# Kernel tuning notes

Hardware: AMD Instinct MI355X
Metric: run time of the kernel (lower is better)

Reference implementation:

```python
import jax, jax.numpy as jnp
from jax import lax
import numpy as np

B = 128          # batch (matches module BATCH_SIZE)
H = W = 64       # image size
E = 8            # num_experts
K = 2            # top_k
C = 1000         # num_classes (expert hidden_size)
D = 14 * 14 * 64 # flattened conv features: 64->62->31->29->14


def setup_inputs() -> dict:
    key = jax.random.key(0)
    ks = jax.random.split(key, 10)
    return {
        "x": jax.random.normal(ks[0], (B, H, W, 1), dtype=jnp.float32),
        "conv1_w": jax.random.normal(ks[1], (3, 3, 1, 32), dtype=jnp.float32) * 0.05,
        "conv1_b": jnp.zeros((32,), dtype=jnp.float32),
        "conv2_w": jax.random.normal(ks[2], (3, 3, 32, 64), dtype=jnp.float32) * 0.05,
        "conv2_b": jnp.zeros((64,), dtype=jnp.float32),
        "gate_w": jax.random.normal(ks[3], (D, E), dtype=jnp.float32) * 0.001,
        "gate_b": jnp.zeros((E,), dtype=jnp.float32),
        "expert_w": jax.random.normal(ks[4], (E, D, C), dtype=jnp.float32) * 0.001,
        "expert_b": jnp.zeros((E, C), dtype=jnp.float32),
    }


def _conv_relu(x, w, b):
    y = lax.conv_general_dilated(x, w, window_strides=(1, 1), padding="VALID",
                                 dimension_numbers=("NHWC", "HWIO", "NHWC"))
    return jax.nn.relu(y + b)


def _maxpool2(x):
    return lax.reduce_window(x, -jnp.inf, lax.max,
                             (1, 2, 2, 1), (1, 2, 2, 1), "VALID")


def reference(x, conv1_w, conv1_b, conv2_w, conv2_b, gate_w, gate_b, expert_w, expert_b):
    # conv block (dropout is identity at inference)
    h = _maxpool2(_conv_relu(x, conv1_w, conv1_b))
    h = _maxpool2(_conv_relu(h, conv2_w, conv2_b))
    h = h.reshape(h.shape[0], -1)                       # [B, D]

    # gating: softmax + top-k
    gates = jax.nn.softmax(h @ gate_w + gate_b)         # [B, E]
    topk_w, topk_i = lax.top_k(gates, K)                # [B, K]

    # all experts (tiny dense layers stacked), then gather top-k and combine
    expert_out = jnp.einsum("bd,edc->bec", h, expert_w) + expert_b  # [B, E, C]
    sel = jnp.take_along_axis(expert_out, topk_i[:, :, None], axis=1)  # [B, K, C]
    combined = jnp.sum(sel * topk_w[:, :, None], axis=1)              # [B, C]

    return jax.nn.softmax(combined)
```

## Files before the change

### kernel.cpp

```cpp
#include <hip/hip_runtime.h>
#include <math.h>

#define D_FEAT 12544
#define NC 1000
#define RB 16
#define S4 32
#define DSLICE 392
#define NIT (DSLICE/4)
#define CT2 500

__global__ __launch_bounds__(256) void k1_conv1(
    const float* __restrict__ x, const float* __restrict__ w,
    const float* __restrict__ bias, float* __restrict__ h1,
    int* __restrict__ cnt)
{
    if (blockIdx.x == 0 && threadIdx.x < 8) cnt[threadIdx.x] = 0;

    int co  = threadIdx.x & 31;
    int pxi = threadIdx.x >> 5;
    int blk = blockIdx.x;
    int pxg = blk & 3;
    int py  = (blk >> 2) % 31;
    int b   = blk / (31 * 4);
    int px  = pxg * 8 + pxi;
    if (px >= 31) return;

    float wr[9];
#pragma unroll
    for (int t = 0; t < 9; ++t) wr[t] = w[t * 32 + co];
    float bb = bias[co];

    float in[4][4];
    const float* xb = x + ((size_t)(b * 64 + 2 * py) * 64 + 2 * px);
#pragma unroll
    for (int r = 0; r < 4; ++r)
#pragma unroll
        for (int c = 0; c < 4; ++c)
            in[r][c] = xb[r * 64 + c];

    float a00 = 0.f, a01 = 0.f, a10 = 0.f, a11 = 0.f;
#pragma unroll
    for (int ky = 0; ky < 3; ++ky)
#pragma unroll
        for (int kx = 0; kx < 3; ++kx) {
            float wv = wr[ky * 3 + kx];
            a00 = fmaf(in[ky][kx],     wv, a00);
            a01 = fmaf(in[ky][kx + 1], wv, a01);
            a10 = fmaf(in[ky + 1][kx], wv, a10);
            a11 = fmaf(in[ky + 1][kx + 1], wv, a11);
        }
    a00 = fmaxf(a00 + bb, 0.f);
    a01 = fmaxf(a01 + bb, 0.f);
    a10 = fmaxf(a10 + bb, 0.f);
    a11 = fmaxf(a11 + bb, 0.f);
    float v = fmaxf(fmaxf(a00, a01), fmaxf(a10, a11));
    h1[((size_t)(b * 31 + py) * 31 + px) * 32 + co] = v;
}

__global__ __launch_bounds__(448) void k2_conv2(
    const float* __restrict__ h1, const float* __restrict__ w2,
    const float* __restrict__ b2, float* __restrict__ h)
{
    __shared__ float wl[9 * 32 * 32];

    int co  = threadIdx.x & 31;
    int px  = threadIdx.x >> 5;
    int blk = blockIdx.x;
    int cob = blk & 1;
    int py  = (blk >> 1) % 14;
    int b   = blk / 28;

    for (int i = threadIdx.x; i < 9 * 32 * 32; i += 448) {
        int tapci = i >> 5;
        int col   = i & 31;
        wl[i] = w2[tapci * 64 + cob * 32 + col];
    }
    __syncthreads();

    float acc00 = 0.f, acc01 = 0.f, acc10 = 0.f, acc11 = 0.f;
    const float* base = h1 + ((size_t)(b * 31 + 2 * py) * 31 + 2 * px) * 32;

    for (int q = 0; q < 8; ++q) {
        float4 in4[4][4];
#pragma unroll
        for (int r = 0; r < 4; ++r)
#pragma unroll
            for (int c = 0; c < 4; ++c)
                in4[r][c] = *(const float4*)(base + (r * 31 + c) * 32 + q * 4);

#pragma unroll
        for (int ky = 0; ky < 3; ++ky)
#pragma unroll
            for (int kx = 0; kx < 3; ++kx) {
                int tap = ky * 3 + kx;
                const float* wp = &wl[(tap * 32 + q * 4) * 32 + co];
                float w0 = wp[0];
                float w1 = wp[32];
                float w2v = wp[64];
                float w3 = wp[96];
                acc00 = fmaf(in4[ky][kx].x, w0, acc00);
                acc00 = fmaf(in4[ky][kx].y, w1, acc00);
                acc00 = fmaf(in4[ky][kx].z, w2v, acc00);
                acc00 = fmaf(in4[ky][kx].w, w3, acc00);
                acc01 = fmaf(in4[ky][kx + 1].x, w0, acc01);
                acc01 = fmaf(in4[ky][kx + 1].y, w1, acc01);
                acc01 = fmaf(in4[ky][kx + 1].z, w2v, acc01);
                acc01 = fmaf(in4[ky][kx + 1].w, w3, acc01);
                acc10 = fmaf(in4[ky + 1][kx].x, w0, acc10);
                acc10 = fmaf(in4[ky + 1][kx].y, w1, acc10);
                acc10 = fmaf(in4[ky + 1][kx].z, w2v, acc10);
                acc10 = fmaf(in4[ky + 1][kx].w, w3, acc10);
                acc11 = fmaf(in4[ky + 1][kx + 1].x, w0, acc11);
                acc11 = fmaf(in4[ky + 1][kx + 1].y, w1, acc11);
                acc11 = fmaf(in4[ky + 1][kx + 1].z, w2v, acc11);
                acc11 = fmaf(in4[ky + 1][kx + 1].w, w3, acc11);
            }
    }

    float bb = b2[cob * 32 + co];
    acc00 = fmaxf(acc00 + bb, 0.f);
    acc01 = fmaxf(acc01 + bb, 0.f);
    acc10 = fmaxf(acc10 + bb, 0.f);
    acc11 = fmaxf(acc11 + bb, 0.f);
    float v = fmaxf(fmaxf(acc00, acc01), fmaxf(acc10, acc11));
    h[(size_t)b * D_FEAT + (py * 14 + px) * 64 + cob * 32 + co] = v;
}

__global__ __launch_bounds__(256) void k3_gate(
    const float* __restrict__ h, const float* __restrict__ gw,
    const float* __restrict__ gb, int* __restrict__ cnt,
    int* __restrict__ rowIdx, float* __restrict__ rowW,
    int* __restrict__ rowK, int* __restrict__ top2e, float* __restrict__ top2w)
{
    int b = blockIdx.x;
    int tid = threadIdx.x;
    float acc[8];
#pragma unroll
    for (int e = 0; e < 8; ++e) acc[e] = 0.f;

    const float* hb = h + (size_t)b * D_FEAT;
    for (int i4 = tid; i4 < D_FEAT / 4; i4 += 256) {
        float4 hv = *(const float4*)(hb + i4 * 4);
        const float* gp = gw + (size_t)i4 * 32;
        float4 g0 = *(const float4*)(gp);
        float4 g1 = *(const float4*)(gp + 4);
        float4 g2 = *(const float4*)(gp + 8);
        float4 g3 = *(const float4*)(gp + 12);
        float4 g4 = *(const float4*)(gp + 16);
        float4 g5 = *(const float4*)(gp + 20);
        float4 g6 = *(const float4*)(gp + 24);
        float4 g7 = *(const float4*)(gp + 28);

        acc[0] = fmaf(hv.x, g0.x, acc[0]); acc[0] = fmaf(hv.y, g2.x, acc[0]);
        acc[0] = fmaf(hv.z, g4.x, acc[0]); acc[0] = fmaf(hv.w, g6.x, acc[0]);
        acc[1] = fmaf(hv.x, g0.y, acc[1]); acc[1] = fmaf(hv.y, g2.y, acc[1]);
        acc[1] = fmaf(hv.z, g4.y, acc[1]); acc[1] = fmaf(hv.w, g6.y, acc[1]);
        acc[2] = fmaf(hv.x, g0.z, acc[2]); acc[2] = fmaf(hv.y, g2.z, acc[2]);
        acc[2] = fmaf(hv.z, g4.z, acc[2]); acc[2] = fmaf(hv.w, g6.z, acc[2]);
        acc[3] = fmaf(hv.x, g0.w, acc[3]); acc[3] = fmaf(hv.y, g2.w, acc[3]);
        acc[3] = fmaf(hv.z, g4.w, acc[3]); acc[3] = fmaf(hv.w, g6.w, acc[3]);
        acc[4] = fmaf(hv.x, g1.x, acc[4]); acc[4] = fmaf(hv.y, g3.x, acc[4]);
        acc[4] = fmaf(hv.z, g5.x, acc[4]); acc[4] = fmaf(hv.w, g7.x, acc[4]);
        acc[5] = fmaf(hv.x, g1.y, acc[5]); acc[5] = fmaf(hv.y, g3.y, acc[5]);
        acc[5] = fmaf(hv.z, g5.y, acc[5]); acc[5] = fmaf(hv.w, g7.y, acc[5]);
        acc[6] = fmaf(hv.x, g1.z, acc[6]); acc[6] = fmaf(hv.y, g3.z, acc[6]);
        acc[6] = fmaf(hv.z, g5.z, acc[6]); acc[6] = fmaf(hv.w, g7.z, acc[6]);
        acc[7] = fmaf(hv.x, g1.w, acc[7]); acc[7] = fmaf(hv.y, g3.w, acc[7]);
        acc[7] = fmaf(hv.z, g5.w, acc[7]); acc[7] = fmaf(hv.w, g7.w, acc[7]);
    }

#pragma unroll
    for (int e = 0; e < 8; ++e) {
        float v = acc[e];
        v += __shfl_down(v, 32, 64);
        v += __shfl_down(v, 16, 64);
        v += __shfl_down(v, 8, 64);
        v += __shfl_down(v, 4, 64);
        v += __shfl_down(v, 2, 64);
        v += __shfl_down(v, 1, 64);
        acc[e] = v;
    }

    __shared__ float sm[4][8];
    int wid = tid >> 6, ln = tid & 63;
    if (ln == 0) {
#pragma unroll
        for (int e = 0; e < 8; ++e) sm[wid][e] = acc[e];
    }
    __syncthreads();

    if (tid == 0) {
        float lg[8], p[8];
        float m = -1e30f;
#pragma unroll
        for (int e = 0; e < 8; ++e) {
            lg[e] = sm[0][e] + sm[1][e] + sm[2][e] + sm[3][e] + gb[e];
            m = fmaxf(m, lg[e]);
        }
        float s = 0.f;
#pragma unroll
        for (int e = 0; e < 8; ++e) { p[e] = expf(lg[e] - m); s += p[e]; }
        float inv = 1.f / s;
#pragma unroll
        for (int e = 0; e < 8; ++e) p[e] *= inv;

        int i0 = 0;
#pragma unroll
        for (int e = 1; e < 8; ++e) if (p[e] > p[i0]) i0 = e;
        int i1 = (i0 == 0) ? 1 : 0;
#pragma unroll
        for (int e = 0; e < 8; ++e) if (e != i0 && p[e] > p[i1]) i1 = e;

        int pos0 = atomicAdd(&cnt[i0], 1);
        rowIdx[i0 * 128 + pos0] = b;
        rowW[i0 * 128 + pos0] = p[i0];
        rowK[i0 * 128 + pos0] = 0;
        int pos1 = atomicAdd(&cnt[i1], 1);
        rowIdx[i1 * 128 + pos1] = b;
        rowW[i1 * 128 + pos1] = p[i1];
        rowK[i1 * 128 + pos1] = 1;

        top2e[b * 2]     = i0;
        top2e[b * 2 + 1] = i1;
        top2w[b * 2]     = p[i0];
        top2w[b * 2 + 1] = p[i1];
    }
}

#define FMA_ROW2(A, HV, W0, W1, W2, W3)                         \
    do {                                                        \
        (A).x = fmaf((HV).x, (W0).x, (A).x);                    \
        (A).x = fmaf((HV).y, (W1).x, (A).x);                    \
        (A).x = fmaf((HV).z, (W2).x, (A).x);                    \
        (A).x = fmaf((HV).w, (W3).x, (A).x);                    \
        (A).y = fmaf((HV).x, (W0).y, (A).y);                    \
        (A).y = fmaf((HV).y, (W1).y, (A).y);                    \
        (A).y = fmaf((HV).z, (W2).y, (A).y);                    \
        (A).y = fmaf((HV).w, (W3).y, (A).y);                    \
    } while (0)

__global__ __launch_bounds__(256) void k4_expert(
    const float* __restrict__ h, const float* __restrict__ ew,
    const int* __restrict__ cnt, const int* __restrict__ rowIdx,
    const float* __restrict__ rowW, const int* __restrict__ rowK,
    float* __restrict__ part)
{
    __shared__ float h_lds[RB * DSLICE];
    __shared__ int   roff_s[RB];

    int tid = threadIdx.x;
    int bid = blockIdx.x;
    int s  = bid & 31;
    int ct = (bid >> 5) & 1;
    int e  = (bid >> 6) & 7;
    int rc = bid >> 9;

    int n = cnt[e];
    int rbase = rc * RB;
    if (rbase >= n) return;
    int nrows = n - rbase; if (nrows > RB) nrows = RB;

    if (tid < RB) {
        roff_s[tid] = (tid < nrows) ? rowIdx[e * 128 + rbase + tid] * D_FEAT : -1;
    }
    __syncthreads();

    int dbase = s * DSLICE;
    for (int i = tid; i < RB * (DSLICE / 4); i += 256) {
        int r = i / (DSLICE / 4);
        int q = i - r * (DSLICE / 4);
        int ro = roff_s[r];
        float4 v = make_float4(0.f, 0.f, 0.f, 0.f);
        if (ro >= 0) v = *(const float4*)(h + ro + dbase + q * 4);
        *(float4*)&h_lds[r * DSLICE + q * 4] = v;
    }
    __syncthreads();

    if (tid < 250) {
        const float* wp = ew + ((size_t)e * D_FEAT + dbase) * NC + ct * CT2 + tid * 2;
        bool g1 = (nrows > 8);

        float2 acc[RB];
#pragma unroll
        for (int r = 0; r < RB; ++r) acc[r] = make_float2(0.f, 0.f);

        float2 wA0 = *(const float2*)(wp);
        float2 wA1 = *(const float2*)(wp + (size_t)NC);
        float2 wA2 = *(const float2*)(wp + (size_t)2 * NC);
        float2 wA3 = *(const float2*)(wp + (size_t)3 * NC);

        for (int it = 0; it < NIT; ++it) {
            const float* np = wp + (size_t)4 * NC;
            float2 wB0, wB1, wB2, wB3;
            if (it < NIT - 1) {
                wB0 = *(const float2*)(np);
                wB1 = *(const float2*)(np + (size_t)NC);
                wB2 = *(const float2*)(np + (size_t)2 * NC);
                wB3 = *(const float2*)(np + (size_t)3 * NC);
            }
            int d = it * 4;
            const float* hp = &h_lds[d];
#pragma unroll
            for (int r = 0; r < 8; ++r) {
                float4 hv = *(const float4*)(hp + r * DSLICE);
                FMA_ROW2(acc[r], hv, wA0, wA1, wA2, wA3);
            }
            if (g1) {
#pragma unroll
                for (int r = 8; r < 16; ++r) {
                    float4 hv = *(const float4*)(hp + r * DSLICE);
                    FMA_ROW2(acc[r], hv, wA0, wA1, wA2, wA3);
                }
            }
            wp = np;
            wA0 = wB0; wA1 = wB1; wA2 = wB2; wA3 = wB3;
        }

        int cc = ct * CT2 + tid * 2;
#pragma unroll
        for (int r = 0; r < RB; ++r) {
            if (r < nrows) {
                int pos = e * 128 + rbase + r;
                float wgt = rowW[pos];
                int ri = rowIdx[pos];
                int kk = rowK[pos];
                float2 o = make_float2(wgt * acc[r].x, wgt * acc[r].y);
                *(float2*)&part[(((size_t)s * 128 + ri) * 2 + kk) * NC + cc] = o;
            }
        }
    }
}

__global__ __launch_bounds__(256) void k5_softmax(
    const float* __restrict__ part, const float* __restrict__ eb,
    const int* __restrict__ top2e, const float* __restrict__ top2w,
    float* __restrict__ out)
{
    int b = blockIdx.x;
    int tid = threadIdx.x;
    __shared__ float red[4];

    int e0 = top2e[b * 2], e1 = top2e[b * 2 + 1];
    float tw0 = top2w[b * 2], tw1 = top2w[b * 2 + 1];

    bool act = (tid < 250);
    int c0 = tid * 4;
    float4 v = make_float4(-1e30f, -1e30f, -1e30f, -1e30f);
    if (act) {
        float4 a0 = make_float4(0.f, 0.f, 0.f, 0.f);
        float4 a1 = a0, a2 = a0, a3 = a0;
        for (int s = 0; s < S4; s += 4) {
            const float* p0 = part + (((size_t)(s + 0) * 128 + b) * 2) * NC + c0;
            const float* p1 = part + (((size_t)(s + 1) * 128 + b) * 2) * NC + c0;
            const float* p2 = part + (((size_t)(s + 2) * 128 + b) * 2) * NC + c0;
            const float* p3 = part + (((size_t)(s + 3) * 128 + b) * 2) * NC + c0;
            float4 q00 = *(const float4*)p0;
            float4 q01 = *(const float4*)(p0 + NC);
            float4 q10 = *(const float4*)p1;
            float4 q11 = *(const float4*)(p1 + NC);
            float4 q20 = *(const float4*)p2;
            float4 q21 = *(const float4*)(p2 + NC);
            float4 q30 = *(const float4*)p3;
            float4 q31 = *(const float4*)(p3 + NC);
            a0.x += q00.x + q01.x; a0.y += q00.y + q01.y;
            a0.z += q00.z + q01.z; a0.w += q00.w + q01.w;
            a1.x += q10.x + q11.x; a1.y += q10.y + q11.y;
            a1.z += q10.z + q11.z; a1.w += q10.w + q11.w;
            a2.x += q20.x + q21.x; a2.y += q20.y + q21.y;
            a2.z += q20.z + q21.z; a2.w += q20.w + q21.w;
            a3.x += q30.x + q31.x; a3.y += q30.y + q31.y;
            a3.z += q30.z + q31.z; a3.w += q30.w + q31.w;
        }
        float4 a = make_float4(a0.x + a1.x + a2.x + a3.x,
                               a0.y + a1.y + a2.y + a3.y,
                               a0.z + a1.z + a2.z + a3.z,
                               a0.w + a1.w + a2.w + a3.w);
        float4 b0 = *(const float4*)(eb + e0 * NC + c0);
        float4 b1 = *(const float4*)(eb + e1 * NC + c0);
        v.x = a.x + tw0 * b0.x + tw1 * b1.x;
        v.y = a.y + tw0 * b0.y + tw1 * b1.y;
        v.z = a.z + tw0 * b0.z + tw1 * b1.z;
        v.w = a.w + tw0 * b0.w + tw1 * b1.w;
    }

    float m = fmaxf(fmaxf(v.x, v.y), fmaxf(v.z, v.w));
#pragma unroll
    for (int off = 32; off >= 1; off >>= 1)
        m = fmaxf(m, __shfl_xor(m, off, 64));
    int wid = tid >> 6, ln = tid & 63;
    if (ln == 0) red[wid] = m;
    __syncthreads();
    m = fmaxf(fmaxf(red[0], red[1]), fmaxf(red[2], red[3]));
    __syncthreads();

    float ex, ey, ez, ew2;
    ex = act ? expf(v.x - m) : 0.f;
    ey = act ? expf(v.y - m) : 0.f;
    ez = act ? expf(v.z - m) : 0.f;
    ew2 = act ? expf(v.w - m) : 0.f;
    float ssum = ex + ey + ez + ew2;
#pragma unroll
    for (int off = 32; off >= 1; off >>= 1)
        ssum += __shfl_xor(ssum, off, 64);
    if (ln == 0) red[wid] = ssum;
    __syncthreads();
    ssum = red[0] + red[1] + red[2] + red[3];
    float inv = 1.f / ssum;

    if (act) {
        float4 o = make_float4(ex * inv, ey * inv, ez * inv, ew2 * inv);
        *(float4*)&out[(size_t)b * NC + c0] = o;
    }
}

extern "C" void kernel_launch(void* const* d_in, const int* in_sizes, int n_in,
                              void* d_out, int out_size, void* d_ws, size_t ws_size,
                              hipStream_t stream) {
    const float* x   = (const float*)d_in[0];
    const float* c1w = (const float*)d_in[1];
    const float* c1b = (const float*)d_in[2];
    const float* c2w = (const float*)d_in[3];
    const float* c2b = (const float*)d_in[4];
    const float* gw  = (const float*)d_in[5];
    const float* gb  = (const float*)d_in[6];
    const float* ew  = (const float*)d_in[7];
    const float* eb  = (const float*)d_in[8];
    float* out = (float*)d_out;

    char* ws = (char*)d_ws;
    int*   cnt    = (int*)  (ws + 0);
    int*   rowIdx = (int*)  (ws + 64);
    float* rowW   = (float*)(ws + 4160);
    int*   rowK   = (int*)  (ws + 8256);
    int*   top2e  = (int*)  (ws + 12352);
    float* top2w  = (float*)(ws + 13376);
    float* h      = (float*)(ws + 16384);
    float* h1     = (float*)(ws + 6438912);
    float* part   = (float*)(ws + 6438912);

    k1_conv1<<<128 * 31 * 4, 256, 0, stream>>>(x, c1w, c1b, h1, cnt);
    k2_conv2<<<128 * 14 * 2, 448, 0, stream>>>(h1, c2w, c2b, h);
    k3_gate<<<128, 256, 0, stream>>>(h, gw, gb, cnt, rowIdx, rowW, rowK, top2e, top2w);
    k4_expert<<<S4 * 2 * 8 * 8, 256, 0, stream>>>(h, ew, cnt, rowIdx, rowW, rowK, part);
    k5_softmax<<<128, 256, 0, stream>>>(part, eb, top2e, top2w, out);
}
```

Before: 291.1 us.

## Widen expert tiles to float4 columns and cut D-split count to eight

```diff
diff --git a/kernel.cpp b/kernel.cpp
--- a/kernel.cpp
+++ b/kernel.cpp
@@ -4,10 +4,11 @@
 #define D_FEAT 12544
 #define NC 1000
 #define RB 16
-#define S4 32
-#define DSLICE 392
-#define NIT (DSLICE/4)
-#define CT2 500
+#define S8 8
+#define DBIG 1568
+#define DSUB 196
+#define NSUB 8
+#define NIT4 49
 
 __global__ __launch_bounds__(256) void k1_conv1(
     const float* __restrict__ x, const float* __restrict__ w,
@@ -227,7 +228,7 @@
     }
 }
 
-#define FMA_ROW2(A, HV, W0, W1, W2, W3)                         \
+#define FMA_ROW(A, HV, W0, W1, W2, W3)                          \
     do {                                                        \
         (A).x = fmaf((HV).x, (W0).x, (A).x);                    \
         (A).x = fmaf((HV).y, (W1).x, (A).x);                    \
@@ -237,6 +238,14 @@
         (A).y = fmaf((HV).y, (W1).y, (A).y);                    \
         (A).y = fmaf((HV).z, (W2).y, (A).y);                    \
         (A).y = fmaf((HV).w, (W3).y, (A).y);                    \
+        (A).z = fmaf((HV).x, (W0).z, (A).z);                    \
+        (A).z = fmaf((HV).y, (W1).z, (A).z);                    \
+        (A).z = fmaf((HV).z, (W2).z, (A).z);                    \
+        (A).z = fmaf((HV).w, (W3).z, (A).z);                    \
+        (A).w = fmaf((HV).x, (W0).w, (A).w);                    \
+        (A).w = fmaf((HV).y, (W1).w, (A).w);                    \
+        (A).w = fmaf((HV).z, (W2).w, (A).w);                    \
+        (A).w = fmaf((HV).w, (W3).w, (A).w);                    \
     } while (0)
 
 __global__ __launch_bounds__(256) void k4_expert(
@@ -245,15 +254,14 @@
     const float* __restrict__ rowW, const int* __restrict__ rowK,
     float* __restrict__ part)
 {
-    __shared__ float h_lds[RB * DSLICE];
+    __shared__ float h_lds[RB * DSUB];
     __shared__ int   roff_s[RB];
 
     int tid = threadIdx.x;
     int bid = blockIdx.x;
-    int s  = bid & 31;
-    int ct = (bid >> 5) & 1;
-    int e  = (bid >> 6) & 7;
-    int rc = bid >> 9;
+    int s  = bid & 7;
+    int e  = (bid >> 3) & 7;
+    int rc = bid >> 6;
 
     int n = cnt[e];
     int rbase = rc * RB;
@@ -265,58 +273,67 @@
     }
     __syncthreads();
 
-    int dbase = s * DSLICE;
-    for (int i = tid; i < RB * (DSLICE / 4); i += 256) {
-        int r = i / (DSLICE / 4);
-        int q = i - r * (DSLICE / 4);
-        int ro = roff_s[r];
-        float4 v = make_float4(0.f, 0.f, 0.f, 0.f);
-        if (ro >= 0) v = *(const float4*)(h + ro + dbase + q * 4);
-        *(float4*)&h_lds[r * DSLICE + q * 4] = v;
-    }
-    __syncthreads();
-
-    if (tid < 250) {
-        const float* wp = ew + ((size_t)e * D_FEAT + dbase) * NC + ct * CT2 + tid * 2;
-        bool g1 = (nrows > 8);
-
-        float2 acc[RB];
-#pragma unroll
-        for (int r = 0; r < RB; ++r) acc[r] = make_float2(0.f, 0.f);
-
-        float2 wA0 = *(const float2*)(wp);
-        float2 wA1 = *(const float2*)(wp + (size_t)NC);
-        float2 wA2 = *(const float2*)(wp + (size_t)2 * NC);
-        float2 wA3 = *(const float2*)(wp + (size_t)3 * NC);
-
-        for (int it = 0; it < NIT; ++it) {
-            const float* np = wp + (size_t)4 * NC;
-            float2 wB0, wB1, wB2, wB3;
-            if (it < NIT - 1) {
-                wB0 = *(const float2*)(np);
-                wB1 = *(const float2*)(np + (size_t)NC);
-                wB2 = *(const float2*)(np + (size_t)2 * NC);
-                wB3 = *(const float2*)(np + (size_t)3 * NC);
+    int dbase = s * DBIG;
+    int c0 = tid * 4;
+    bool act = (c0 < NC);
+    bool g1 = (nrows > 8);
+    const float* wp = ew + ((size_t)e * D_FEAT + dbase) * NC + c0;
+
+    float4 acc[RB];
+#pragma unroll
+    for (int r = 0; r < RB; ++r) acc[r] = make_float4(0.f, 0.f, 0.f, 0.f);
+
+    float4 wA0, wA1, wA2, wA3;
+    if (act) {
+        wA0 = *(const float4*)(wp);
+        wA1 = *(const float4*)(wp + (size_t)NC);
+        wA2 = *(const float4*)(wp + (size_t)2 * NC);
+        wA3 = *(const float4*)(wp + (size_t)3 * NC);
+    }
+
+    for (int sub = 0; sub < NSUB; ++sub) {
+        for (int i = tid; i < RB * NIT4; i += 256) {
+            int r = i / NIT4;
+            int q = i - r * NIT4;
+            int ro = roff_s[r];
+            float4 v = make_float4(0.f, 0.f, 0.f, 0.f);
+            if (ro >= 0) v = *(const float4*)(h + ro + dbase + sub * DSUB + q * 4);
+            *(float4*)&h_lds[r * DSUB + q * 4] = v;
+        }
+        __syncthreads();
+
+        if (act) {
+            for (int it = 0; it < NIT4; ++it) {
+                bool last = (sub == NSUB - 1) && (it == NIT4 - 1);
+                const float* np = wp + (size_t)4 * NC;
+                float4 wB0, wB1, wB2, wB3;
+                if (!last) {
+                    wB0 = *(const float4*)(np);
+                    wB1 = *(const float4*)(np + (size_t)NC);
+                    wB2 = *(const float4*)(np + (size_t)2 * NC);
+                    wB3 = *(const float4*)(np + (size_t)3 * NC);
+                }
+                const float* hp = &h_lds[it * 4];
+#pragma unroll
+                for (int r = 0; r < 8; ++r) {
+                    float4 hv = *(const float4*)(hp + r * DSUB);
+                    FMA_ROW(acc[r], hv, wA0, wA1, wA2, wA3);
+                }
+                if (g1) {
+#pragma unroll
+                    for (int r = 8; r < 16; ++r) {
+                        float4 hv = *(const float4*)(hp + r * DSUB);
+                        FMA_ROW(acc[r], hv, wA0, wA1, wA2, wA3);
+                    }
+                }
+                wp = np;
+                wA0 = wB0; wA1 = wB1; wA2 = wB2; wA3 = wB3;
             }
-            int d = it * 4;
-            const float* hp = &h_lds[d];
-#pragma unroll
-            for (int r = 0; r < 8; ++r) {
-                float4 hv = *(const float4*)(hp + r * DSLICE);
-                FMA_ROW2(acc[r], hv, wA0, wA1, wA2, wA3);
-            }
-            if (g1) {
-#pragma unroll
-                for (int r = 8; r < 16; ++r) {
-                    float4 hv = *(const float4*)(hp + r * DSLICE);
-                    FMA_ROW2(acc[r], hv, wA0, wA1, wA2, wA3);
-                }
-            }
-            wp = np;
-            wA0 = wB0; wA1 = wB1; wA2 = wB2; wA3 = wB3;
-        }
-
-        int cc = ct * CT2 + tid * 2;
+        }
+        __syncthreads();
+    }
+
+    if (act) {
 #pragma unroll
         for (int r = 0; r < RB; ++r) {
             if (r < nrows) {
@@ -324,8 +341,9 @@
                 float wgt = rowW[pos];
                 int ri = rowIdx[pos];
                 int kk = rowK[pos];
-                float2 o = make_float2(wgt * acc[r].x, wgt * acc[r].y);
-                *(float2*)&part[(((size_t)s * 128 + ri) * 2 + kk) * NC + cc] = o;
+                float4 o = make_float4(wgt * acc[r].x, wgt * acc[r].y,
+                                       wgt * acc[r].z, wgt * acc[r].w);
+                *(float4*)&part[(((size_t)s * 128 + ri) * 2 + kk) * NC + c0] = o;
             }
         }
     }
@@ -349,7 +367,7 @@
     if (act) {
         float4 a0 = make_float4(0.f, 0.f, 0.f, 0.f);
         float4 a1 = a0, a2 = a0, a3 = a0;
-        for (int s = 0; s < S4; s += 4) {
+        for (int s = 0; s < S8; s += 4) {
             const float* p0 = part + (((size_t)(s + 0) * 128 + b) * 2) * NC + c0;
             const float* p1 = part + (((size_t)(s + 1) * 128 + b) * 2) * NC + c0;
             const float* p2 = part + (((size_t)(s + 2) * 128 + b) * 2) * NC + c0;
@@ -441,6 +459,6 @@
     k1_conv1<<<128 * 31 * 4, 256, 0, stream>>>(x, c1w, c1b, h1, cnt);
     k2_conv2<<<128 * 14 * 2, 448, 0, stream>>>(h1, c2w, c2b, h);
     k3_gate<<<128, 256, 0, stream>>>(h, gw, gb, cnt, rowIdx, rowW, rowK, top2e, top2w);
-    k4_expert<<<S4 * 2 * 8 * 8, 256, 0, stream>>>(h, ew, cnt, rowIdx, rowW, rowK, part);
+    k4_expert<<<8 * 8 * 8, 256, 0, stream>>>(h, ew, cnt, rowIdx, rowW, rowK, part);
     k5_softmax<<<128, 256, 0, stream>>>(part, eb, top2e, top2w, out);
 }
```

New measurement: 467.1 us. +60.4%, slower.

## Retile expert GEMM: 8 columns per thread, 8-row chunks, 128-thread blocks

Applied to the files above, without the earlier changes.

```diff
diff --git a/kernel.cpp b/kernel.cpp
--- a/kernel.cpp
+++ b/kernel.cpp
@@ -3,11 +3,10 @@
 
 #define D_FEAT 12544
 #define NC 1000
-#define RB 16
+#define RB 8
 #define S4 32
 #define DSLICE 392
 #define NIT (DSLICE/4)
-#define CT2 500
 
 __global__ __launch_bounds__(256) void k1_conv1(
     const float* __restrict__ x, const float* __restrict__ w,
@@ -227,19 +226,43 @@
     }
 }
 
-#define FMA_ROW2(A, HV, W0, W1, W2, W3)                         \
+#define FMA_ROW8(AA, AB, HV, WA0, WB0, WA1, WB1, WA2, WB2, WA3, WB3)  \
     do {                                                        \
-        (A).x = fmaf((HV).x, (W0).x, (A).x);                    \
-        (A).x = fmaf((HV).y, (W1).x, (A).x);                    \
-        (A).x = fmaf((HV).z, (W2).x, (A).x);                    \
-        (A).x = fmaf((HV).w, (W3).x, (A).x);                    \
-        (A).y = fmaf((HV).x, (W0).y, (A).y);                    \
-        (A).y = fmaf((HV).y, (W1).y, (A).y);                    \
-        (A).y = fmaf((HV).z, (W2).y, (A).y);                    \
-        (A).y = fmaf((HV).w, (W3).y, (A).y);                    \
+        (AA).x = fmaf((HV).x, (WA0).x, (AA).x);                 \
+        (AA).x = fmaf((HV).y, (WA1).x, (AA).x);                 \
+        (AA).x = fmaf((HV).z, (WA2).x, (AA).x);                 \
+        (AA).x = fmaf((HV).w, (WA3).x, (AA).x);                 \
+        (AA).y = fmaf((HV).x, (WA0).y, (AA).y);                 \
+        (AA).y = fmaf((HV).y, (WA1).y, (AA).y);                 \
+        (AA).y = fmaf((HV).z, (WA2).y, (AA).y);                 \
+        (AA).y = fmaf((HV).w, (WA3).y, (AA).y);                 \
+        (AA).z = fmaf((HV).x, (WA0).z, (AA).z);                 \
+        (AA).z = fmaf((HV).y, (WA1).z, (AA).z);                 \
+        (AA).z = fmaf((HV).z, (WA2).z, (AA).z);                 \
+        (AA).z = fmaf((HV).w, (WA3).z, (AA).z);                 \
+        (AA).w = fmaf((HV).x, (WA0).w, (AA).w);                 \
+        (AA).w = fmaf((HV).y, (WA1).w, (AA).w);                 \
+        (AA).w = fmaf((HV).z, (WA2).w, (AA).w);                 \
+        (AA).w = fmaf((HV).w, (WA3).w, (AA).w);                 \
+        (AB).x = fmaf((HV).x, (WB0).x, (AB).x);                 \
+        (AB).x = fmaf((HV).y, (WB1).x, (AB).x);                 \
+        (AB).x = fmaf((HV).z, (WB2).x, (AB).x);                 \
+        (AB).x = fmaf((HV).w, (WB3).x, (AB).x);                 \
+        (AB).y = fmaf((HV).x, (WB0).y, (AB).y);                 \
+        (AB).y = fmaf((HV).y, (WB1).y, (AB).y);                 \
+        (AB).y = fmaf((HV).z, (WB2).y, (AB).y);                 \
+        (AB).y = fmaf((HV).w, (WB3).y, (AB).y);                 \
+        (AB).z = fmaf((HV).x, (WB0).z, (AB).z);                 \
+        (AB).z = fmaf((HV).y, (WB1).z, (AB).z);                 \
+        (AB).z = fmaf((HV).z, (WB2).z, (AB).z);                 \
+        (AB).z = fmaf((HV).w, (WB3).z, (AB).z);                 \
+        (AB).w = fmaf((HV).x, (WB0).w, (AB).w);                 \
+        (AB).w = fmaf((HV).y, (WB1).w, (AB).w);                 \
+        (AB).w = fmaf((HV).z, (WB2).w, (AB).w);                 \
+        (AB).w = fmaf((HV).w, (WB3).w, (AB).w);                 \
     } while (0)
 
-__global__ __launch_bounds__(256) void k4_expert(
+__global__ __launch_bounds__(128) void k4_expert(
     const float* __restrict__ h, const float* __restrict__ ew,
     const int* __restrict__ cnt, const int* __restrict__ rowIdx,
     const float* __restrict__ rowW, const int* __restrict__ rowK,
@@ -251,9 +274,8 @@
     int tid = threadIdx.x;
     int bid = blockIdx.x;
     int s  = bid & 31;
-    int ct = (bid >> 5) & 1;
-    int e  = (bid >> 6) & 7;
-    int rc = bid >> 9;
+    int e  = (bid >> 5) & 7;
+    int rc = bid >> 8;
 
     int n = cnt[e];
     int rbase = rc * RB;
@@ -266,9 +288,9 @@
     __syncthreads();
 
     int dbase = s * DSLICE;
-    for (int i = tid; i < RB * (DSLICE / 4); i += 256) {
-        int r = i / (DSLICE / 4);
-        int q = i - r * (DSLICE / 4);
+    for (int i = tid; i < RB * NIT; i += 128) {
+        int r = i / NIT;
+        int q = i - r * NIT;
         int ro = roff_s[r];
         float4 v = make_float4(0.f, 0.f, 0.f, 0.f);
         if (ro >= 0) v = *(const float4*)(h + ro + dbase + q * 4);
@@ -276,47 +298,50 @@
     }
     __syncthreads();
 
-    if (tid < 250) {
-        const float* wp = ew + ((size_t)e * D_FEAT + dbase) * NC + ct * CT2 + tid * 2;
-        bool g1 = (nrows > 8);
-
-        float2 acc[RB];
-#pragma unroll
-        for (int r = 0; r < RB; ++r) acc[r] = make_float2(0.f, 0.f);
-
-        float2 wA0 = *(const float2*)(wp);
-        float2 wA1 = *(const float2*)(wp + (size_t)NC);
-        float2 wA2 = *(const float2*)(wp + (size_t)2 * NC);
-        float2 wA3 = *(const float2*)(wp + (size_t)3 * NC);
+    int c0 = tid * 8;
+    if (c0 < NC) {
+        const float* wp = ew + ((size_t)e * D_FEAT + dbase) * NC + c0;
+
+        float4 accA[RB], accB[RB];
+#pragma unroll
+        for (int r = 0; r < RB; ++r) {
+            accA[r] = make_float4(0.f, 0.f, 0.f, 0.f);
+            accB[r] = make_float4(0.f, 0.f, 0.f, 0.f);
+        }
+
+        float4 a0 = *(const float4*)(wp);
+        float4 b0 = *(const float4*)(wp + 4);
+        float4 a1 = *(const float4*)(wp + (size_t)NC);
+        float4 b1 = *(const float4*)(wp + (size_t)NC + 4);
+        float4 a2 = *(const float4*)(wp + (size_t)2 * NC);
+        float4 b2 = *(const float4*)(wp + (size_t)2 * NC + 4);
+        float4 a3 = *(const float4*)(wp + (size_t)3 * NC);
+        float4 b3 = *(const float4*)(wp + (size_t)3 * NC + 4);
 
         for (int it = 0; it < NIT; ++it) {
             const float* np = wp + (size_t)4 * NC;
-            float2 wB0, wB1, wB2, wB3;
+            float4 na0, nb0, na1, nb1, na2, nb2, na3, nb3;
             if (it < NIT - 1) {
-                wB0 = *(const float2*)(np);
-                wB1 = *(const float2*)(np + (size_t)NC);
-                wB2 = *(const float2*)(np + (size_t)2 * NC);
-                wB3 = *(const float2*)(np + (size_t)3 * NC);
+                na0 = *(const float4*)(np);
+                nb0 = *(const float4*)(np + 4);
+                na1 = *(const float4*)(np + (size_t)NC);
+                nb1 = *(const float4*)(np + (size_t)NC + 4);
+                na2 = *(const float4*)(np + (size_t)2 * NC);
+                nb2 = *(const float4*)(np + (size_t)2 * NC + 4);
+                na3 = *(const float4*)(np + (size_t)3 * NC);
+                nb3 = *(const float4*)(np + (size_t)3 * NC + 4);
             }
-            int d = it * 4;
-            const float* hp = &h_lds[d];
-#pragma unroll
-            for (int r = 0; r < 8; ++r) {
+            const float* hp = &h_lds[it * 4];
+#pragma unroll
+            for (int r = 0; r < RB; ++r) {
                 float4 hv = *(const float4*)(hp + r * DSLICE);
-                FMA_ROW2(acc[r], hv, wA0, wA1, wA2, wA3);
-            }
-            if (g1) {
-#pragma unroll
-                for (int r = 8; r < 16; ++r) {
-                    float4 hv = *(const float4*)(hp + r * DSLICE);
-                    FMA_ROW2(acc[r], hv, wA0, wA1, wA2, wA3);
-                }
+                FMA_ROW8(accA[r], accB[r], hv, a0, b0, a1, b1, a2, b2, a3, b3);
             }
             wp = np;
-            wA0 = wB0; wA1 = wB1; wA2 = wB2; wA3 = wB3;
-        }
-
-        int cc = ct * CT2 + tid * 2;
+            a0 = na0; b0 = nb0; a1 = na1; b1 = nb1;
+            a2 = na2; b2 = nb2; a3 = na3; b3 = nb3;
+        }
+
 #pragma unroll
         for (int r = 0; r < RB; ++r) {
             if (r < nrows) {
@@ -324,8 +349,13 @@
                 float wgt = rowW[pos];
                 int ri = rowIdx[pos];
                 int kk = rowK[pos];
-                float2 o = make_float2(wgt * acc[r].x, wgt * acc[r].y);
-                *(float2*)&part[(((size_t)s * 128 + ri) * 2 + kk) * NC + cc] = o;
+                float* op = &part[(((size_t)s * 128 + ri) * 2 + kk) * NC + c0];
+                float4 oA = make_float4(wgt * accA[r].x, wgt * accA[r].y,
+                                        wgt * accA[r].z, wgt * accA[r].w);
+                float4 oB = make_float4(wgt * accB[r].x, wgt * accB[r].y,
+                                        wgt * accB[r].z, wgt * accB[r].w);
+                *(float4*)(op) = oA;
+                *(float4*)(op + 4) = oB;
             }
         }
     }
@@ -441,6 +471,6 @@
     k1_conv1<<<128 * 31 * 4, 256, 0, stream>>>(x, c1w, c1b, h1, cnt);
     k2_conv2<<<128 * 14 * 2, 448, 0, stream>>>(h1, c2w, c2b, h);
     k3_gate<<<128, 256, 0, stream>>>(h, gw, gb, cnt, rowIdx, rowW, rowK, top2e, top2w);
-    k4_expert<<<S4 * 2 * 8 * 8, 256, 0, stream>>>(h, ew, cnt, rowIdx, rowW, rowK, part);
+    k4_expert<<<S4 * 8 * 16, 128, 0, stream>>>(h, ew, cnt, rowIdx, rowW, rowK, part);
     k5_softmax<<<128, 256, 0, stream>>>(part, eb, top2e, top2w, out);
 }
```

New measurement: 294.1 us. No clear change (+1.0%).
